# Optimization experiments

Hardware: AMD Instinct MI355X
Metric: run time of the kernel (lower is better)

Reference implementation:

```python
import jax, jax.numpy as jnp
import numpy as np

NUM_HEADS = 16


def setup_inputs() -> dict:
    key = jax.random.key(0)
    k1, k2, k3, k4, k5 = jax.random.split(key, 5)
    B, S, D = 4, 2048, 1024
    hidden_states = jax.random.normal(k1, (B, S, D), dtype=jnp.float32)
    c_attn_w = jax.random.normal(k2, (D, 3 * D), dtype=jnp.float32) * 0.02
    c_attn_b = jax.random.normal(k3, (3 * D,), dtype=jnp.float32) * 0.02
    c_proj_w = jax.random.normal(k4, (D, D), dtype=jnp.float32) * 0.02
    c_proj_b = jax.random.normal(k5, (D,), dtype=jnp.float32) * 0.02
    return {
        "hidden_states": hidden_states,
        "c_attn_w": c_attn_w,
        "c_attn_b": c_attn_b,
        "c_proj_w": c_proj_w,
        "c_proj_b": c_proj_b,
    }


def reference(hidden_states, c_attn_w, c_attn_b, c_proj_w, c_proj_b):
    B, S, D = hidden_states.shape
    H = NUM_HEADS
    Dh = D // H

    # fused QKV projection (Conv1D: x @ W + b)
    qkv = hidden_states @ c_attn_w + c_attn_b          # [B, S, 3D]
    q, k, v = jnp.split(qkv, 3, axis=-1)

    def split_heads(t):
        return t.reshape(B, S, H, Dh).transpose(0, 2, 1, 3)  # [B, H, S, Dh]

    q, k, v = split_heads(q), split_heads(k), split_heads(v)

    # scaled dot-product attention with causal mask (eager GPT2 _attn)
    scores = jnp.einsum("bhqd,bhkd->bhqk", q, k) / jnp.asarray(Dh ** 0.5, q.dtype)
    causal = jnp.tril(jnp.ones((S, S), dtype=bool))
    mask_value = jnp.finfo(scores.dtype).min
    scores = jnp.where(causal[None, None], scores, mask_value)
    probs = jax.nn.softmax(scores, axis=-1)            # attn_pdrop=0 -> no dropout
    attn = jnp.einsum("bhqk,bhkd->bhqd", probs, v)     # [B, H, S, Dh]

    # merge heads + output projection (resid_pdrop=0)
    attn = attn.transpose(0, 2, 1, 3).reshape(B, S, D)
    out = attn @ c_proj_w + c_proj_b
    return out
```

## Files before the change

kernel.cpp:

```cpp
#include <hip/hip_runtime.h>
#include <hip/hip_bf16.h>
#include <stdint.h>

typedef __bf16 bf16_t;
typedef __bf16 bf16x8 __attribute__((ext_vector_type(8)));
typedef __bf16 bf16x4 __attribute__((ext_vector_type(4)));
typedef float f32x4 __attribute__((ext_vector_type(4)));
typedef float f32x16 __attribute__((ext_vector_type(16)));

#define B_ 4
#define S_ 2048
#define D_ 1024
#define H_ 16
#define DH_ 64

__global__ __launch_bounds__(256) void cast_f32_to_bf16(const float* __restrict__ in,
                                                        bf16_t* __restrict__ out, int n4) {
  int i = blockIdx.x * 256 + threadIdx.x;
  if (i < n4) {
    const float4 v = reinterpret_cast<const float4*>(in)[i];
    bf16x4 o;
    o[0] = (bf16_t)v.x; o[1] = (bf16_t)v.y; o[2] = (bf16_t)v.z; o[3] = (bf16_t)v.w;
    reinterpret_cast<bf16x4*>(out)[i] = o;
  }
}

__global__ __launch_bounds__(256) void transpose_cast(const float* __restrict__ in,
                                                      bf16_t* __restrict__ out, int K, int N) {
  __shared__ float tile[32][33];
  const int bx = blockIdx.x * 32;
  const int by = blockIdx.y * 32;
  const int tx = threadIdx.x & 31;
  const int ty = threadIdx.x >> 5;
#pragma unroll
  for (int i = 0; i < 32; i += 8)
    tile[ty + i][tx] = in[(size_t)(by + ty + i) * N + bx + tx];
  __syncthreads();
#pragma unroll
  for (int i = 0; i < 32; i += 8)
    out[(size_t)(bx + ty + i) * K + by + tx] = (bf16_t)tile[tx][ty + i];
}

__device__ __forceinline__ void gload_lds16(const bf16_t* g, bf16_t* l) {
  __builtin_amdgcn_global_load_lds((const __attribute__((address_space(1))) void*)g,
                                   (__attribute__((address_space(3))) void*)l, 16, 0, 0);
}

template <int MODE>
__global__ __launch_bounds__(256) void gemm_bf16_128(
    const bf16_t* __restrict__ A, const bf16_t* __restrict__ Bt,
    const float* __restrict__ bias,
    bf16_t* __restrict__ Qb, bf16_t* __restrict__ Kb, bf16_t* __restrict__ Vtb,
    float* __restrict__ Out, int M, int N, int K) {
  __shared__ alignas(16) bf16_t As[128 * 32];
  __shared__ alignas(16) bf16_t Bs[128 * 32];
  const int t = threadIdx.x;
  const int wave = t >> 6, lane = t & 63;
  const int r = lane & 15, g = lane >> 4;
  const int bm = blockIdx.x, bn = blockIdx.y;
  const int wm = (wave & 1) * 64, wn = (wave >> 1) * 64;

  f32x4 acc[4][4];
#pragma unroll
  for (int i = 0; i < 4; ++i)
#pragma unroll
    for (int j = 0; j < 4; ++j) acc[i][j] = f32x4{0.f, 0.f, 0.f, 0.f};

  const int c0 = t;
  const int c1 = t + 256;

  for (int kk = 0; kk < K; kk += 32) {
    __syncthreads();
    gload_lds16(A + (size_t)(bm * 128 + (c0 >> 2)) * K + kk + (c0 & 3) * 8,
                As + (size_t)(wave * 64) * 8);
    gload_lds16(A + (size_t)(bm * 128 + (c1 >> 2)) * K + kk + (c1 & 3) * 8,
                As + (size_t)(256 + wave * 64) * 8);
    gload_lds16(Bt + (size_t)(bn * 128 + (c0 >> 2)) * K + kk + (c0 & 3) * 8,
                Bs + (size_t)(wave * 64) * 8);
    gload_lds16(Bt + (size_t)(bn * 128 + (c1 >> 2)) * K + kk + (c1 & 3) * 8,
                Bs + (size_t)(256 + wave * 64) * 8);
    __syncthreads();

    bf16x8 af[4], bfr[4];
#pragma unroll
    for (int f = 0; f < 4; ++f)
      af[f] = *reinterpret_cast<const bf16x8*>(&As[(wm + 16 * f + r) * 32 + g * 8]);
#pragma unroll
    for (int f = 0; f < 4; ++f)
      bfr[f] = *reinterpret_cast<const bf16x8*>(&Bs[(wn + 16 * f + r) * 32 + g * 8]);
#pragma unroll
    for (int fm = 0; fm < 4; ++fm)
#pragma unroll
      for (int fn = 0; fn < 4; ++fn)
        acc[fm][fn] =
            __builtin_amdgcn_mfma_f32_16x16x32_bf16(af[fm], bfr[fn], acc[fm][fn], 0, 0, 0);
  }

  const int row0 = bm * 128 + wm + g * 4;
  const int col0 = bn * 128 + wn + r;
#pragma unroll
  for (int fn = 0; fn < 4; ++fn) {
    const int col = col0 + 16 * fn;
    const float bv = bias[col];
    if (MODE == 0) {
      const int part = col >> 10, w = col & 1023;
      const int h = w >> 6, dh = w & 63;
#pragma unroll
      for (int fm = 0; fm < 4; ++fm)
#pragma unroll
        for (int j = 0; j < 4; ++j) {
          const int row = row0 + 16 * fm + j;
          const int b = row >> 11, s = row & 2047;
          const float val = acc[fm][fn][j] + bv;
          const size_t bhb = (size_t)(b * H_ + h);
          if (part == 0) {
            Qb[(bhb * S_ + s) * DH_ + dh] = (bf16_t)val;
          } else if (part == 1) {
            Kb[(bhb * S_ + s) * DH_ + dh] = (bf16_t)val;
          } else {
            Vtb[(bhb * DH_ + dh) * S_ + s] = (bf16_t)val;
          }
        }
    } else {
#pragma unroll
      for (int fm = 0; fm < 4; ++fm)
#pragma unroll
        for (int j = 0; j < 4; ++j) {
          const int row = row0 + 16 * fm + j;
          Out[(size_t)row * N + col] = acc[fm][fn][j] + bv;
        }
    }
  }
}

__global__ __launch_bounds__(256) void attn_flash3(const bf16_t* __restrict__ Qb,
                                                   const bf16_t* __restrict__ Kb,
                                                   const bf16_t* __restrict__ Vtb,
                                                   bf16_t* __restrict__ attnb) {
  __shared__ alignas(16) bf16_t Kl[2][64 * 64];
  __shared__ alignas(16) bf16_t Vl[2][64 * 64];
  __shared__ alignas(16) bf16_t Ps[4][32 * 72];
  const int t = threadIdx.x, wave = t >> 6, lane = t & 63;
  const int q5 = lane & 31, hi = lane >> 5;
  const int bh = blockIdx.x, pair = blockIdx.y;
  const size_t kqbase = (size_t)bh * (S_ * DH_);
  const size_t vbase = (size_t)bh * (DH_ * S_);
  const int b = bh >> 4, h = bh & 15;
  const float SC = 0.18033688f;

  const int r0s = t >> 3, ch0 = t & 7;
  const int r1s = (t + 256) >> 3, ch1 = t & 7;
  const int lk0 = r0s * 64 + ((ch0 ^ (r0s & 7)) << 3);
  const int lk1 = r1s * 64 + ((ch1 ^ (r1s & 7)) << 3);

  for (int pass = 0; pass < 2; ++pass) {
    const int qb = pass ? 15 - pair : pair;
    const int qbase = qb * 128;
    const int wq = qbase + wave * 32;
    const int qg = wq + q5;
    const int ktmax = 2 * qb + 1;
    const int ktw = wq >> 6;

    bf16x8 qf[4];
#pragma unroll
    for (int d = 0; d < 4; ++d)
      qf[d] = *reinterpret_cast<const bf16x8*>(Qb + kqbase + (size_t)qg * DH_ + d * 16 + hi * 8);

    f32x16 oa, ob;
#pragma unroll
    for (int r = 0; r < 16; ++r) { oa[r] = 0.f; ob[r] = 0.f; }
    float mrun = -1e30f, lrun = 0.f;

    {
      const bf16_t* kg = Kb + kqbase;
      const bf16_t* vg = Vtb + vbase;
      const uint4 a = *reinterpret_cast<const uint4*>(kg + r0s * DH_ + ch0 * 8);
      const uint4 bq = *reinterpret_cast<const uint4*>(kg + r1s * DH_ + ch1 * 8);
      const uint4 c = *reinterpret_cast<const uint4*>(vg + (size_t)r0s * S_ + ch0 * 8);
      const uint4 d = *reinterpret_cast<const uint4*>(vg + (size_t)r1s * S_ + ch1 * 8);
      *reinterpret_cast<uint4*>(&Kl[0][lk0]) = a;
      *reinterpret_cast<uint4*>(&Kl[0][lk1]) = bq;
      *reinterpret_cast<uint4*>(&Vl[0][lk0]) = c;
      *reinterpret_cast<uint4*>(&Vl[0][lk1]) = d;
      __syncthreads();
    }

    int cur = 0;
    for (int kt = 0; kt <= ktmax; ++kt) {
      uint4 ra, rb, rc, rd;
      const bool more = kt < ktmax;
      if (more) {
        const bf16_t* kg = Kb + kqbase + (size_t)(kt + 1) * (64 * DH_);
        const bf16_t* vg = Vtb + vbase + (kt + 1) * 64;
        ra = *reinterpret_cast<const uint4*>(kg + r0s * DH_ + ch0 * 8);
        rb = *reinterpret_cast<const uint4*>(kg + r1s * DH_ + ch1 * 8);
        rc = *reinterpret_cast<const uint4*>(vg + (size_t)r0s * S_ + ch0 * 8);
        rd = *reinterpret_cast<const uint4*>(vg + (size_t)r1s * S_ + ch1 * 8);
      }

      if (kt <= ktw) {
        const bf16_t* KL = &Kl[cur][0];
        const bf16_t* VL = &Vl[cur][0];
        f32x16 s0, s1;
#pragma unroll
        for (int r = 0; r < 16; ++r) { s0[r] = 0.f; s1[r] = 0.f; }
#pragma unroll
        for (int d = 0; d < 4; ++d) {
          const int cx = ((2 * d + hi) ^ (q5 & 7)) << 3;
          const bf16x8 kfa = *reinterpret_cast<const bf16x8*>(&KL[q5 * 64 + cx]);
          s0 = __builtin_amdgcn_mfma_f32_32x32x16_bf16(kfa, qf[d], s0, 0, 0, 0);
          const bf16x8 kfb = *reinterpret_cast<const bf16x8*>(&KL[(32 + q5) * 64 + cx]);
          s1 = __builtin_amdgcn_mfma_f32_32x32x16_bf16(kfb, qf[d], s1, 0, 0, 0);
        }

        float p0[16], p1[16];
#pragma unroll
        for (int r = 0; r < 16; ++r) { p0[r] = s0[r] * SC; p1[r] = s1[r] * SC; }
        if (kt == ktw) {
#pragma unroll
          for (int r = 0; r < 16; ++r) {
            const int crow = (r & 3) + 8 * (r >> 2) + 4 * hi;
            if (kt * 64 + crow > qg) p0[r] = -1e30f;
            if (kt * 64 + 32 + crow > qg) p1[r] = -1e30f;
          }
        }

        float t8[8];
#pragma unroll
        for (int i = 0; i < 8; ++i)
          t8[i] = fmaxf(fmaxf(p0[i], p0[i + 8]), fmaxf(p1[i], p1[i + 8]));
        float vm = fmaxf(fmaxf(fmaxf(t8[0], t8[1]), fmaxf(t8[2], t8[3])),
                         fmaxf(fmaxf(t8[4], t8[5]), fmaxf(t8[6], t8[7])));
        vm = fmaxf(vm, __shfl_xor(vm, 32));
        const float mnew = fmaxf(mrun, vm);
        const float fac = exp2f(mrun - mnew);
#pragma unroll
        for (int r = 0; r < 16; ++r) {
          p0[r] = exp2f(p0[r] - mnew);
          p1[r] = exp2f(p1[r] - mnew);
        }
        float s8[8];
#pragma unroll
        for (int i = 0; i < 8; ++i) s8[i] = (p0[i] + p0[i + 8]) + (p1[i] + p1[i + 8]);
        float sum = ((s8[0] + s8[1]) + (s8[2] + s8[3])) + ((s8[4] + s8[5]) + (s8[6] + s8[7]));
        sum += __shfl_xor(sum, 32);
        lrun = lrun * fac + sum;
        mrun = mnew;
#pragma unroll
        for (int r = 0; r < 16; ++r) { oa[r] *= fac; ob[r] *= fac; }

        bf16_t* PSW = &Ps[wave][0];
#pragma unroll
        for (int r = 0; r < 16; r += 2) {
          const int crow = (r & 3) + 8 * (r >> 2) + 4 * hi;
          union { bf16_t hh[2]; unsigned u; } ua, ub;
          ua.hh[0] = (bf16_t)p0[r]; ua.hh[1] = (bf16_t)p0[r + 1];
          ub.hh[0] = (bf16_t)p1[r]; ub.hh[1] = (bf16_t)p1[r + 1];
          *reinterpret_cast<unsigned*>(&PSW[q5 * 72 + crow]) = ua.u;
          *reinterpret_cast<unsigned*>(&PSW[q5 * 72 + 32 + crow]) = ub.u;
        }

#pragma unroll
        for (int tt = 0; tt < 4; ++tt) {
          const bf16x8 pb = *reinterpret_cast<const bf16x8*>(&PSW[q5 * 72 + tt * 16 + hi * 8]);
          const int cx = ((2 * tt + hi) ^ (q5 & 7)) << 3;
          const bf16x8 va = *reinterpret_cast<const bf16x8*>(&VL[q5 * 64 + cx]);
          oa = __builtin_amdgcn_mfma_f32_32x32x16_bf16(va, pb, oa, 0, 0, 0);
          const bf16x8 vb = *reinterpret_cast<const bf16x8*>(&VL[(32 + q5) * 64 + cx]);
          ob = __builtin_amdgcn_mfma_f32_32x32x16_bf16(vb, pb, ob, 0, 0, 0);
        }
      }

      if (more) {
        *reinterpret_cast<uint4*>(&Kl[cur ^ 1][lk0]) = ra;
        *reinterpret_cast<uint4*>(&Kl[cur ^ 1][lk1]) = rb;
        *reinterpret_cast<uint4*>(&Vl[cur ^ 1][lk0]) = rc;
        *reinterpret_cast<uint4*>(&Vl[cur ^ 1][lk1]) = rd;
      }
      __syncthreads();
      cur ^= 1;
    }

    const float inv = 1.0f / lrun;
    bf16_t* PSW = &Ps[wave][0];
#pragma unroll
    for (int r = 0; r < 16; ++r) {
      const int crow = (r & 3) + 8 * (r >> 2) + 4 * hi;
      PSW[q5 * 72 + crow] = (bf16_t)(oa[r] * inv);
      PSW[q5 * 72 + 32 + crow] = (bf16_t)(ob[r] * inv);
    }
#pragma unroll
    for (int i = 0; i < 4; ++i) {
      const int cc = i * 64 + lane;
      const int row = cc >> 3, ch = cc & 7;
      const bf16x8 v = *reinterpret_cast<const bf16x8*>(&PSW[row * 72 + ch * 8]);
      *reinterpret_cast<bf16x8*>(attnb + ((size_t)(b * S_ + wq + row)) * D_ + h * DH_ + ch * 8) = v;
    }
  }
}

extern "C" void kernel_launch(void* const* d_in, const int* in_sizes, int n_in, void* d_out,
                              int out_size, void* d_ws, size_t ws_size, hipStream_t stream) {
  const float* x = (const float*)d_in[0];
  const float* wqkv = (const float*)d_in[1];
  const float* bqkv = (const float*)d_in[2];
  const float* wproj = (const float*)d_in[3];
  const float* bproj = (const float*)d_in[4];
  float* out = (float*)d_out;
  char* ws = (char*)d_ws;

  bf16_t* xb = (bf16_t*)(ws);
  bf16_t* wqkvT = (bf16_t*)(ws + 16777216);
  bf16_t* wprojT = (bf16_t*)(ws + 23068672);
  bf16_t* Qb = (bf16_t*)(ws + 25165824);
  bf16_t* Kb = (bf16_t*)(ws + 41943040);
  bf16_t* Vtb = (bf16_t*)(ws + 58720256);
  bf16_t* attnb = (bf16_t*)(ws + 75497472);

  cast_f32_to_bf16<<<8192, 256, 0, stream>>>(x, xb, (8192 * 1024) / 4);
  transpose_cast<<<dim3(96, 32), 256, 0, stream>>>(wqkv, wqkvT, 1024, 3072);
  transpose_cast<<<dim3(32, 32), 256, 0, stream>>>(wproj, wprojT, 1024, 1024);
  gemm_bf16_128<0><<<dim3(64, 24), 256, 0, stream>>>(xb, wqkvT, bqkv, Qb, Kb, Vtb, nullptr,
                                                     8192, 3072, 1024);
  attn_flash3<<<dim3(64, 8), 256, 0, stream>>>(Qb, Kb, Vtb, attnb);
  gemm_bf16_128<1><<<dim3(64, 8), 256, 0, stream>>>(attnb, wprojT, bproj, nullptr, nullptr,
                                                    nullptr, out, 8192, 1024, 1024);
}
```

Baseline: 296.7 us.

## One q-block per attention workgroup, lazy softmax rescale, vectorized V-transpose stores

```diff
diff --git a/kernel.cpp b/kernel.cpp
--- a/kernel.cpp
+++ b/kernel.cpp
@@ -106,21 +106,22 @@
       const int part = col >> 10, w = col & 1023;
       const int h = w >> 6, dh = w & 63;
 #pragma unroll
-      for (int fm = 0; fm < 4; ++fm)
-#pragma unroll
-        for (int j = 0; j < 4; ++j) {
-          const int row = row0 + 16 * fm + j;
-          const int b = row >> 11, s = row & 2047;
-          const float val = acc[fm][fn][j] + bv;
-          const size_t bhb = (size_t)(b * H_ + h);
-          if (part == 0) {
-            Qb[(bhb * S_ + s) * DH_ + dh] = (bf16_t)val;
-          } else if (part == 1) {
-            Kb[(bhb * S_ + s) * DH_ + dh] = (bf16_t)val;
-          } else {
-            Vtb[(bhb * DH_ + dh) * S_ + s] = (bf16_t)val;
-          }
+      for (int fm = 0; fm < 4; ++fm) {
+        const int row = row0 + 16 * fm;
+        const int b = row >> 11, s = row & 2047;
+        const size_t bhb = (size_t)(b * H_ + h);
+        if (part == 2) {
+          union { bf16_t hh[4]; uint2 u; } pk;
+#pragma unroll
+          for (int j = 0; j < 4; ++j) pk.hh[j] = (bf16_t)(acc[fm][fn][j] + bv);
+          *reinterpret_cast<uint2*>(&Vtb[(bhb * DH_ + dh) * S_ + s]) = pk.u;
+        } else {
+          bf16_t* dst = (part == 0) ? Qb : Kb;
+#pragma unroll
+          for (int j = 0; j < 4; ++j)
+            dst[(bhb * S_ + s + j) * DH_ + dh] = (bf16_t)(acc[fm][fn][j] + bv);
         }
+      }
     } else {
 #pragma unroll
       for (int fm = 0; fm < 4; ++fm)
@@ -133,7 +134,7 @@
   }
 }
 
-__global__ __launch_bounds__(256) void attn_flash3(const bf16_t* __restrict__ Qb,
+__global__ __launch_bounds__(256) void attn_flash4(const bf16_t* __restrict__ Qb,
                                                    const bf16_t* __restrict__ Kb,
                                                    const bf16_t* __restrict__ Vtb,
                                                    bf16_t* __restrict__ attnb) {
@@ -142,7 +143,7 @@
   __shared__ alignas(16) bf16_t Ps[4][32 * 72];
   const int t = threadIdx.x, wave = t >> 6, lane = t & 63;
   const int q5 = lane & 31, hi = lane >> 5;
-  const int bh = blockIdx.x, pair = blockIdx.y;
+  const int bh = blockIdx.x, qb = 15 - (int)blockIdx.y;
   const size_t kqbase = (size_t)bh * (S_ * DH_);
   const size_t vbase = (size_t)bh * (DH_ * S_);
   const int b = bh >> 4, h = bh & 15;
@@ -153,149 +154,150 @@
   const int lk0 = r0s * 64 + ((ch0 ^ (r0s & 7)) << 3);
   const int lk1 = r1s * 64 + ((ch1 ^ (r1s & 7)) << 3);
 
-  for (int pass = 0; pass < 2; ++pass) {
-    const int qb = pass ? 15 - pair : pair;
-    const int qbase = qb * 128;
-    const int wq = qbase + wave * 32;
-    const int qg = wq + q5;
-    const int ktmax = 2 * qb + 1;
-    const int ktw = wq >> 6;
-
-    bf16x8 qf[4];
-#pragma unroll
-    for (int d = 0; d < 4; ++d)
-      qf[d] = *reinterpret_cast<const bf16x8*>(Qb + kqbase + (size_t)qg * DH_ + d * 16 + hi * 8);
-
-    f32x16 oa, ob;
-#pragma unroll
-    for (int r = 0; r < 16; ++r) { oa[r] = 0.f; ob[r] = 0.f; }
-    float mrun = -1e30f, lrun = 0.f;
-
-    {
-      const bf16_t* kg = Kb + kqbase;
-      const bf16_t* vg = Vtb + vbase;
-      const uint4 a = *reinterpret_cast<const uint4*>(kg + r0s * DH_ + ch0 * 8);
-      const uint4 bq = *reinterpret_cast<const uint4*>(kg + r1s * DH_ + ch1 * 8);
-      const uint4 c = *reinterpret_cast<const uint4*>(vg + (size_t)r0s * S_ + ch0 * 8);
-      const uint4 d = *reinterpret_cast<const uint4*>(vg + (size_t)r1s * S_ + ch1 * 8);
-      *reinterpret_cast<uint4*>(&Kl[0][lk0]) = a;
-      *reinterpret_cast<uint4*>(&Kl[0][lk1]) = bq;
-      *reinterpret_cast<uint4*>(&Vl[0][lk0]) = c;
-      *reinterpret_cast<uint4*>(&Vl[0][lk1]) = d;
-      __syncthreads();
+  const int qbase = qb * 128;
+  const int wq = qbase + wave * 32;
+  const int qg = wq + q5;
+  const int ktmax = 2 * qb + 1;
+  const int ktw = wq >> 6;
+
+  bf16x8 qf[4];
+#pragma unroll
+  for (int d = 0; d < 4; ++d)
+    qf[d] = *reinterpret_cast<const bf16x8*>(Qb + kqbase + (size_t)qg * DH_ + d * 16 + hi * 8);
+
+  f32x16 oa, ob;
+#pragma unroll
+  for (int r = 0; r < 16; ++r) { oa[r] = 0.f; ob[r] = 0.f; }
+  float mrun = -1e30f, lrun = 0.f;
+
+  {
+    const bf16_t* kg = Kb + kqbase;
+    const bf16_t* vg = Vtb + vbase;
+    const uint4 a = *reinterpret_cast<const uint4*>(kg + r0s * DH_ + ch0 * 8);
+    const uint4 bq = *reinterpret_cast<const uint4*>(kg + r1s * DH_ + ch1 * 8);
+    const uint4 c = *reinterpret_cast<const uint4*>(vg + (size_t)r0s * S_ + ch0 * 8);
+    const uint4 d = *reinterpret_cast<const uint4*>(vg + (size_t)r1s * S_ + ch1 * 8);
+    *reinterpret_cast<uint4*>(&Kl[0][lk0]) = a;
+    *reinterpret_cast<uint4*>(&Kl[0][lk1]) = bq;
+    *reinterpret_cast<uint4*>(&Vl[0][lk0]) = c;
+    *reinterpret_cast<uint4*>(&Vl[0][lk1]) = d;
+    __syncthreads();
+  }
+
+  int cur = 0;
+  for (int kt = 0; kt <= ktmax; ++kt) {
+    uint4 ra, rb, rc, rd;
+    const bool more = kt < ktmax;
+    if (more) {
+      const bf16_t* kg = Kb + kqbase + (size_t)(kt + 1) * (64 * DH_);
+      const bf16_t* vg = Vtb + vbase + (kt + 1) * 64;
+      ra = *reinterpret_cast<const uint4*>(kg + r0s * DH_ + ch0 * 8);
+      rb = *reinterpret_cast<const uint4*>(kg + r1s * DH_ + ch1 * 8);
+      rc = *reinterpret_cast<const uint4*>(vg + (size_t)r0s * S_ + ch0 * 8);
+      rd = *reinterpret_cast<const uint4*>(vg + (size_t)r1s * S_ + ch1 * 8);
     }
 
-    int cur = 0;
-    for (int kt = 0; kt <= ktmax; ++kt) {
-      uint4 ra, rb, rc, rd;
-      const bool more = kt < ktmax;
-      if (more) {
-        const bf16_t* kg = Kb + kqbase + (size_t)(kt + 1) * (64 * DH_);
-        const bf16_t* vg = Vtb + vbase + (kt + 1) * 64;
-        ra = *reinterpret_cast<const uint4*>(kg + r0s * DH_ + ch0 * 8);
-        rb = *reinterpret_cast<const uint4*>(kg + r1s * DH_ + ch1 * 8);
-        rc = *reinterpret_cast<const uint4*>(vg + (size_t)r0s * S_ + ch0 * 8);
-        rd = *reinterpret_cast<const uint4*>(vg + (size_t)r1s * S_ + ch1 * 8);
-      }
-
-      if (kt <= ktw) {
-        const bf16_t* KL = &Kl[cur][0];
-        const bf16_t* VL = &Vl[cur][0];
-        f32x16 s0, s1;
-#pragma unroll
-        for (int r = 0; r < 16; ++r) { s0[r] = 0.f; s1[r] = 0.f; }
-#pragma unroll
-        for (int d = 0; d < 4; ++d) {
-          const int cx = ((2 * d + hi) ^ (q5 & 7)) << 3;
-          const bf16x8 kfa = *reinterpret_cast<const bf16x8*>(&KL[q5 * 64 + cx]);
-          s0 = __builtin_amdgcn_mfma_f32_32x32x16_bf16(kfa, qf[d], s0, 0, 0, 0);
-          const bf16x8 kfb = *reinterpret_cast<const bf16x8*>(&KL[(32 + q5) * 64 + cx]);
-          s1 = __builtin_amdgcn_mfma_f32_32x32x16_bf16(kfb, qf[d], s1, 0, 0, 0);
+    if (kt <= ktw) {
+      const bf16_t* KL = &Kl[cur][0];
+      const bf16_t* VL = &Vl[cur][0];
+      f32x16 s0, s1;
+#pragma unroll
+      for (int r = 0; r < 16; ++r) { s0[r] = 0.f; s1[r] = 0.f; }
+#pragma unroll
+      for (int d = 0; d < 4; ++d) {
+        const int cx = ((2 * d + hi) ^ (q5 & 7)) << 3;
+        const bf16x8 kfa = *reinterpret_cast<const bf16x8*>(&KL[q5 * 64 + cx]);
+        s0 = __builtin_amdgcn_mfma_f32_32x32x16_bf16(kfa, qf[d], s0, 0, 0, 0);
+        const bf16x8 kfb = *reinterpret_cast<const bf16x8*>(&KL[(32 + q5) * 64 + cx]);
+        s1 = __builtin_amdgcn_mfma_f32_32x32x16_bf16(kfb, qf[d], s1, 0, 0, 0);
+      }
+
+      if (kt == ktw) {
+#pragma unroll
+        for (int r = 0; r < 16; ++r) {
+          const int crow = (r & 3) + 8 * (r >> 2) + 4 * hi;
+          if (kt * 64 + crow > qg) s0[r] = -1e30f;
+          if (kt * 64 + 32 + crow > qg) s1[r] = -1e30f;
         }
-
-        float p0[16], p1[16];
-#pragma unroll
-        for (int r = 0; r < 16; ++r) { p0[r] = s0[r] * SC; p1[r] = s1[r] * SC; }
-        if (kt == ktw) {
-#pragma unroll
-          for (int r = 0; r < 16; ++r) {
-            const int crow = (r & 3) + 8 * (r >> 2) + 4 * hi;
-            if (kt * 64 + crow > qg) p0[r] = -1e30f;
-            if (kt * 64 + 32 + crow > qg) p1[r] = -1e30f;
-          }
-        }
-
-        float t8[8];
-#pragma unroll
-        for (int i = 0; i < 8; ++i)
-          t8[i] = fmaxf(fmaxf(p0[i], p0[i + 8]), fmaxf(p1[i], p1[i + 8]));
-        float vm = fmaxf(fmaxf(fmaxf(t8[0], t8[1]), fmaxf(t8[2], t8[3])),
-                         fmaxf(fmaxf(t8[4], t8[5]), fmaxf(t8[6], t8[7])));
-        vm = fmaxf(vm, __shfl_xor(vm, 32));
-        const float mnew = fmaxf(mrun, vm);
+      }
+
+      float t8[8];
+#pragma unroll
+      for (int i = 0; i < 8; ++i)
+        t8[i] = fmaxf(fmaxf(s0[i], s0[i + 8]), fmaxf(s1[i], s1[i + 8]));
+      float vm = fmaxf(fmaxf(fmaxf(t8[0], t8[1]), fmaxf(t8[2], t8[3])),
+                       fmaxf(fmaxf(t8[4], t8[5]), fmaxf(t8[6], t8[7])));
+      vm = fmaxf(vm, __shfl_xor(vm, 32));
+      const float vms = vm * SC;
+
+      if (!__all(vms - mrun <= 8.f)) {
+        const float mnew = fmaxf(mrun, vms);
         const float fac = exp2f(mrun - mnew);
 #pragma unroll
-        for (int r = 0; r < 16; ++r) {
-          p0[r] = exp2f(p0[r] - mnew);
-          p1[r] = exp2f(p1[r] - mnew);
-        }
-        float s8[8];
-#pragma unroll
-        for (int i = 0; i < 8; ++i) s8[i] = (p0[i] + p0[i + 8]) + (p1[i] + p1[i + 8]);
-        float sum = ((s8[0] + s8[1]) + (s8[2] + s8[3])) + ((s8[4] + s8[5]) + (s8[6] + s8[7]));
-        sum += __shfl_xor(sum, 32);
-        lrun = lrun * fac + sum;
+        for (int r = 0; r < 16; ++r) { oa[r] *= fac; ob[r] *= fac; }
+        lrun *= fac;
         mrun = mnew;
-#pragma unroll
-        for (int r = 0; r < 16; ++r) { oa[r] *= fac; ob[r] *= fac; }
-
-        bf16_t* PSW = &Ps[wave][0];
-#pragma unroll
-        for (int r = 0; r < 16; r += 2) {
-          const int crow = (r & 3) + 8 * (r >> 2) + 4 * hi;
-          union { bf16_t hh[2]; unsigned u; } ua, ub;
-          ua.hh[0] = (bf16_t)p0[r]; ua.hh[1] = (bf16_t)p0[r + 1];
-          ub.hh[0] = (bf16_t)p1[r]; ub.hh[1] = (bf16_t)p1[r + 1];
-          *reinterpret_cast<unsigned*>(&PSW[q5 * 72 + crow]) = ua.u;
-          *reinterpret_cast<unsigned*>(&PSW[q5 * 72 + 32 + crow]) = ub.u;
-        }
-
-#pragma unroll
-        for (int tt = 0; tt < 4; ++tt) {
-          const bf16x8 pb = *reinterpret_cast<const bf16x8*>(&PSW[q5 * 72 + tt * 16 + hi * 8]);
-          const int cx = ((2 * tt + hi) ^ (q5 & 7)) << 3;
-          const bf16x8 va = *reinterpret_cast<const bf16x8*>(&VL[q5 * 64 + cx]);
-          oa = __builtin_amdgcn_mfma_f32_32x32x16_bf16(va, pb, oa, 0, 0, 0);
-          const bf16x8 vb = *reinterpret_cast<const bf16x8*>(&VL[(32 + q5) * 64 + cx]);
-          ob = __builtin_amdgcn_mfma_f32_32x32x16_bf16(vb, pb, ob, 0, 0, 0);
-        }
-      }
-
-      if (more) {
-        *reinterpret_cast<uint4*>(&Kl[cur ^ 1][lk0]) = ra;
-        *reinterpret_cast<uint4*>(&Kl[cur ^ 1][lk1]) = rb;
-        *reinterpret_cast<uint4*>(&Vl[cur ^ 1][lk0]) = rc;
-        *reinterpret_cast<uint4*>(&Vl[cur ^ 1][lk1]) = rd;
-      }
-      __syncthreads();
-      cur ^= 1;
+      }
+
+      float p0[16], p1[16];
+#pragma unroll
+      for (int r = 0; r < 16; ++r) {
+        p0[r] = exp2f(fmaf(s0[r], SC, -mrun));
+        p1[r] = exp2f(fmaf(s1[r], SC, -mrun));
+      }
+      float s8[8];
+#pragma unroll
+      for (int i = 0; i < 8; ++i) s8[i] = (p0[i] + p0[i + 8]) + (p1[i] + p1[i + 8]);
+      float sum = ((s8[0] + s8[1]) + (s8[2] + s8[3])) + ((s8[4] + s8[5]) + (s8[6] + s8[7]));
+      sum += __shfl_xor(sum, 32);
+      lrun += sum;
+
+      bf16_t* PSW = &Ps[wave][0];
+#pragma unroll
+      for (int r = 0; r < 16; r += 2) {
+        const int crow = (r & 3) + 8 * (r >> 2) + 4 * hi;
+        union { bf16_t hh[2]; unsigned u; } ua, ub;
+        ua.hh[0] = (bf16_t)p0[r]; ua.hh[1] = (bf16_t)p0[r + 1];
+        ub.hh[0] = (bf16_t)p1[r]; ub.hh[1] = (bf16_t)p1[r + 1];
+        *reinterpret_cast<unsigned*>(&PSW[q5 * 72 + crow]) = ua.u;
+        *reinterpret_cast<unsigned*>(&PSW[q5 * 72 + 32 + crow]) = ub.u;
+      }
+
+#pragma unroll
+      for (int tt = 0; tt < 4; ++tt) {
+        const bf16x8 pb = *reinterpret_cast<const bf16x8*>(&PSW[q5 * 72 + tt * 16 + hi * 8]);
+        const int cx = ((2 * tt + hi) ^ (q5 & 7)) << 3;
+        const bf16x8 va = *reinterpret_cast<const bf16x8*>(&VL[q5 * 64 + cx]);
+        oa = __builtin_amdgcn_mfma_f32_32x32x16_bf16(va, pb, oa, 0, 0, 0);
+        const bf16x8 vb = *reinterpret_cast<const bf16x8*>(&VL[(32 + q5) * 64 + cx]);
+        ob = __builtin_amdgcn_mfma_f32_32x32x16_bf16(vb, pb, ob, 0, 0, 0);
+      }
     }
 
-    const float inv = 1.0f / lrun;
-    bf16_t* PSW = &Ps[wave][0];
-#pragma unroll
-    for (int r = 0; r < 16; ++r) {
-      const int crow = (r & 3) + 8 * (r >> 2) + 4 * hi;
-      PSW[q5 * 72 + crow] = (bf16_t)(oa[r] * inv);
-      PSW[q5 * 72 + 32 + crow] = (bf16_t)(ob[r] * inv);
+    if (more) {
+      *reinterpret_cast<uint4*>(&Kl[cur ^ 1][lk0]) = ra;
+      *reinterpret_cast<uint4*>(&Kl[cur ^ 1][lk1]) = rb;
+      *reinterpret_cast<uint4*>(&Vl[cur ^ 1][lk0]) = rc;
+      *reinterpret_cast<uint4*>(&Vl[cur ^ 1][lk1]) = rd;
     }
-#pragma unroll
-    for (int i = 0; i < 4; ++i) {
-      const int cc = i * 64 + lane;
-      const int row = cc >> 3, ch = cc & 7;
-      const bf16x8 v = *reinterpret_cast<const bf16x8*>(&PSW[row * 72 + ch * 8]);
-      *reinterpret_cast<bf16x8*>(attnb + ((size_t)(b * S_ + wq + row)) * D_ + h * DH_ + ch * 8) = v;
-    }
+    __syncthreads();
+    cur ^= 1;
+  }
+
+  const float inv = 1.0f / lrun;
+  bf16_t* PSW = &Ps[wave][0];
+#pragma unroll
+  for (int r = 0; r < 16; ++r) {
+    const int crow = (r & 3) + 8 * (r >> 2) + 4 * hi;
+    PSW[q5 * 72 + crow] = (bf16_t)(oa[r] * inv);
+    PSW[q5 * 72 + 32 + crow] = (bf16_t)(ob[r] * inv);
+  }
+#pragma unroll
+  for (int i = 0; i < 4; ++i) {
+    const int cc = i * 64 + lane;
+    const int row = cc >> 3, ch = cc & 7;
+    const bf16x8 v = *reinterpret_cast<const bf16x8*>(&PSW[row * 72 + ch * 8]);
+    *reinterpret_cast<bf16x8*>(attnb + ((size_t)(b * S_ + wq + row)) * D_ + h * DH_ + ch * 8) = v;
   }
 }
 
@@ -322,7 +324,7 @@
   transpose_cast<<<dim3(32, 32), 256, 0, stream>>>(wproj, wprojT, 1024, 1024);
   gemm_bf16_128<0><<<dim3(64, 24), 256, 0, stream>>>(xb, wqkvT, bqkv, Qb, Kb, Vtb, nullptr,
                                                      8192, 3072, 1024);
-  attn_flash3<<<dim3(64, 8), 256, 0, stream>>>(Qb, Kb, Vtb, attnb);
+  attn_flash4<<<dim3(64, 16), 256, 0, stream>>>(Qb, Kb, Vtb, attnb);
   gemm_bf16_128<1><<<dim3(64, 8), 256, 0, stream>>>(attnb, wprojT, bproj, nullptr, nullptr,
                                                     nullptr, out, 8192, 1024, 1024);
 }
```

Result: faster. 279.4 us (-5.8%).
